# Kernel optimization log

Hardware: AMD Instinct MI355X
Metric: run time of the kernel (lower is better)

The kernel has to match this reference:

```python
import jax, jax.numpy as jnp
import numpy as np

N_NODES = 100000
N_EDGES = 1600000
MUL = 32            # channel multiplicity for every irrep
INV_SQRT_MUL = 1.0 / np.sqrt(32.0)
# path constants: wigner-3j norms (1/sqrt3 for 0x1->1 and 1x1->0, 1/sqrt6 for 1x1->1)
# combined with fan-in path normalization (fan=32 for 0e out, fan=64 for 1o out, 2 paths)
C_DOT = 1.0 / np.sqrt(3.0 * 32.0)
C_SCL = 1.0 / np.sqrt(3.0 * 64.0)
C_CRS = 1.0 / np.sqrt(6.0 * 64.0)


def setup_inputs() -> dict:
    key = jax.random.key(0)
    ks = jax.random.split(key, 12)
    x = jax.random.normal(ks[0], (N_NODES, 128), jnp.float32)
    pos = jax.random.normal(ks[1], (N_NODES, 3), jnp.float32)
    edge_index = jax.random.randint(ks[2], (2, N_EDGES), 0, N_NODES, jnp.int32)
    # o3.Linear(32x0e+32x1o -> 32x0e+32x0e+32x1o): per-irrep channel mixing
    W_node_s = jax.random.normal(ks[3], (32, 64), jnp.float32)   # 0e -> (scalars|gates)
    W_node_v = jax.random.normal(ks[4], (32, 32), jnp.float32)   # 1o -> 1o
    # FullyConnectedTensorProduct(32x0e+32x1o, 1x1o -> 32x0e+32x1o): 3 CG paths
    W_tp_d = jax.random.normal(ks[5], (32, 32), jnp.float32)     # 1o x 1o -> 0e (dot)
    W_tp_s = jax.random.normal(ks[6], (32, 32), jnp.float32)     # 0e x 1o -> 1o
    W_tp_c = jax.random.normal(ks[7], (32, 32), jnp.float32)     # 1o x 1o -> 1o (cross)
    # o3.Linear(32x0e+32x1o -> 32x0e+32x1o)
    W_msg_s = jax.random.normal(ks[8], (32, 32), jnp.float32)
    W_msg_v = jax.random.normal(ks[9], (32, 32), jnp.float32)
    ln_gamma = jnp.ones((128,), jnp.float32)
    ln_beta = jnp.zeros((128,), jnp.float32)
    return {"x": x, "pos": pos, "edge_index": edge_index,
            "W_node_s": W_node_s, "W_node_v": W_node_v,
            "W_tp_d": W_tp_d, "W_tp_s": W_tp_s, "W_tp_c": W_tp_c,
            "W_msg_s": W_msg_s, "W_msg_v": W_msg_v,
            "ln_gamma": ln_gamma, "ln_beta": ln_beta}


def reference(x, pos, edge_index, W_node_s, W_node_v, W_tp_d, W_tp_s, W_tp_c,
              W_msg_s, W_msg_v, ln_gamma, ln_beta):
    N = x.shape[0]
    row, col = edge_index[0], edge_index[1]
    # split node irreps: 32 scalars (0e) | 32 vectors (1o) of dim 3
    s = x[:, :32]                       # [N,32]
    v = x[:, 32:].reshape(-1, 32, 3)    # [N,32,3]
    # lin_node (equivariant linear, path-normalized by 1/sqrt(fan_in)=1/sqrt(32))
    h_s = (s @ W_node_s) * INV_SQRT_MUL                          # [N,64]
    h_v = jnp.einsum('nid,ij->njd', v, W_node_v) * INV_SQRT_MUL  # [N,32,3]
    # Gate: relu scalars, sigmoid gates multiply the gated vectors
    sc = jax.nn.relu(h_s[:, :32])                                # [N,32]
    hv = h_v * jax.nn.sigmoid(h_s[:, 32:])[:, :, None]           # [N,32,3]
    # spherical harmonics l=1, component norm: sqrt(3)*unit vec in e3nn (y,z,x) order
    rel = pos[col] - pos[row]                                    # [E,3]
    unit = rel / jnp.sqrt(jnp.sum(rel * rel, -1, keepdims=True) + 1e-12)
    u = jnp.sqrt(3.0) * unit[:, (1, 2, 0)]                       # [E,3]
    # gather source-node features per edge
    sj = sc[col]                                                 # [E,32]
    vj = hv[col]                                                 # [E,32,3]
    # CG tensor product paths
    dot = jnp.einsum('eid,ed->ei', vj, u)                        # 1o x 1o -> 0e
    crs = jnp.cross(vj, u[:, None, :])                           # 1o x 1o -> 1o
    m0 = (dot @ W_tp_d) * C_DOT                                  # [E,32]
    m1 = (sj @ W_tp_s)[:, :, None] * u[:, None, :] * C_SCL \
         + jnp.einsum('eid,ik->ekd', crs, W_tp_c) * C_CRS        # [E,32,3]
    m = jnp.concatenate([m0, m1.reshape(-1, 96)], -1)            # [E,128]
    # scatter-mean over destination nodes (row)
    deg = jax.ops.segment_sum(jnp.ones_like(row, jnp.float32), row,
                              num_segments=N).clip(1.0)
    mi = jax.ops.segment_sum(m, row, num_segments=N) / deg[:, None]
    # lin_msg
    ms = (mi[:, :32] @ W_msg_s) * INV_SQRT_MUL
    mv = jnp.einsum('nid,ij->njd', mi[:, 32:].reshape(-1, 32, 3),
                    W_msg_v) * INV_SQRT_MUL
    o = jnp.concatenate([ms, mv.reshape(-1, 96)], -1)            # [N,128]
    # LayerNorm over 128 dims (as in the original, affine)
    mu = o.mean(-1, keepdims=True)
    var = o.var(-1, keepdims=True)
    o = (o - mu) / jnp.sqrt(var + 1e-5) * ln_gamma + ln_beta
    return x + o
```

## Files before the change

kernel.cpp:

```cpp
#include <hip/hip_runtime.h>
#include <math.h>


static constexpr float INV_SQRT_MUL = 0.17677669529663687f;
static constexpr float C_DOT = 0.10206207261596575f;
static constexpr float C_SCL = 0.07216878364870322f;
static constexpr float C_CRS = 0.05103103630798288f;
static constexpr float SQRT3 = 1.7320508075688772f;
static constexpr int MAXDEG = 48;

#define WS_ALIGN(x) (((x) + 255) & ~(size_t)255)

__device__ __forceinline__ unsigned short f2bf(float v) {
    unsigned int b = __float_as_uint(v);
    b += 0x7FFFu + ((b >> 16) & 1u);
    return (unsigned short)(b >> 16);
}
__device__ __forceinline__ float bf2f(unsigned short u) {
    return __uint_as_float(((unsigned int)u) << 16);
}

__global__ __launch_bounds__(1024)
void fuse_weights(const float* __restrict__ Wtpd, const float* __restrict__ Wtps,
                  const float* __restrict__ Wtpc, const float* __restrict__ Wms,
                  const float* __restrict__ Wmv,
                  float* __restrict__ Wds, float* __restrict__ Wsv, float* __restrict__ Wcv) {
    int t = threadIdx.x;
    int i = t >> 5, j = t & 31;
    float a = 0.f, b = 0.f, c = 0.f;
#pragma unroll
    for (int k = 0; k < 32; ++k) {
        a += Wtpd[i * 32 + k] * Wms[k * 32 + j];
        b += Wtps[i * 32 + k] * Wmv[k * 32 + j];
        c += Wtpc[i * 32 + k] * Wmv[k * 32 + j];
    }
    Wds[t] = a * (C_DOT * INV_SQRT_MUL);
    Wsv[t] = b * (C_SCL * INV_SQRT_MUL);
    Wcv[t] = c * (C_CRS * INV_SQRT_MUL);
}

__global__ __launch_bounds__(128)
void node_feat_scatter(const float* __restrict__ x, const float* __restrict__ Wns,
                       const float* __restrict__ Wnv, unsigned short* __restrict__ feat,
                       const int* __restrict__ eidx, int* __restrict__ cnt,
                       int* __restrict__ slots, int N, int E) {
    int t = threadIdx.x;
    float w[32], wg[32];
    int d = 0, pidx;
    if (t < 32) {
        pidx = t * 4;
#pragma unroll
        for (int k = 0; k < 32; ++k) w[k] = Wns[k * 64 + t];
    } else {
        int cc = t - 32; d = cc >> 5; int i = cc & 31;
        pidx = i * 4 + 1 + d;
#pragma unroll
        for (int k = 0; k < 32; ++k) { w[k] = Wnv[k * 32 + i]; wg[k] = Wns[k * 64 + 32 + i]; }
    }
    __shared__ float xs[128];
    for (int n = blockIdx.x; n < N; n += gridDim.x) {
        xs[t] = x[(size_t)n * 128 + t];
        __syncthreads();
        float val;
        if (t < 32) {
            float h = 0.f;
#pragma unroll
            for (int k = 0; k < 32; ++k) h += xs[k] * w[k];
            val = fmaxf(h * INV_SQRT_MUL, 0.f);
        } else {
            float h = 0.f, g = 0.f;
#pragma unroll
            for (int k = 0; k < 32; ++k) { h += xs[32 + k * 3 + d] * w[k]; g += xs[k] * wg[k]; }
            float sig = 1.f / (1.f + expf(-g * INV_SQRT_MUL));
            val = h * INV_SQRT_MUL * sig;
        }
        feat[(size_t)n * 128 + pidx] = f2bf(val);
        __syncthreads();
    }
    for (int e = blockIdx.x * 128 + t; e < E; e += gridDim.x * 128) {
        int r = eidx[e];
        int c = eidx[E + e];
        int p = atomicAdd(&cnt[r], 1);
        if (p < MAXDEG) __builtin_nontemporal_store(c, &slots[(size_t)r * MAXDEG + p]);
    }
}

__global__ __launch_bounds__(256)
void agg_kernel(const float* __restrict__ x, const float* __restrict__ pos,
                const ushort4* __restrict__ feat, const int* __restrict__ cnt,
                const int* __restrict__ slots,
                const float* __restrict__ Wds, const float* __restrict__ Wsv,
                const float* __restrict__ Wcv, const float* __restrict__ gamma,
                const float* __restrict__ beta, float* __restrict__ out, int N) {
    int t = threadIdx.x;
    int hw = t >> 5;
    int lane = t & 31;
    int n = blockIdx.x * 8 + hw;
    bool live = (n < N);

    __shared__ float4 cu[8][MAXDEG];
    __shared__ float4 finA[8][32];
    __shared__ float4 finB[8][32];

    int deg = live ? cnt[n] : 0;
    int c = min(deg, MAXDEG);

    float prx = 0.f, pry = 0.f, prz = 0.f;
    if (live) { prx = pos[n * 3 + 0]; pry = pos[n * 3 + 1]; prz = pos[n * 3 + 2]; }

    if (lane < c) {
        int col = slots[(size_t)n * MAXDEG + lane];
        float rx = pos[col * 3 + 0] - prx;
        float ry = pos[col * 3 + 1] - pry;
        float rz = pos[col * 3 + 2] - prz;
        float inv = rsqrtf(rx * rx + ry * ry + rz * rz + 1e-12f) * SQRT3;
        cu[hw][lane] = make_float4(ry * inv, rz * inv, rx * inv, __int_as_float(col));
    }
    if (c > 32 && lane < c - 32) {
        int col = slots[(size_t)n * MAXDEG + 32 + lane];
        float rx = pos[col * 3 + 0] - prx;
        float ry = pos[col * 3 + 1] - pry;
        float rz = pos[col * 3 + 2] - prz;
        float inv = rsqrtf(rx * rx + ry * ry + rz * rz + 1e-12f) * SQRT3;
        cu[hw][32 + lane] = make_float4(ry * inv, rz * inv, rx * inv, __int_as_float(col));
    }
    __syncthreads();

    float D = 0.f, S0 = 0.f, S1 = 0.f, S2 = 0.f, C0 = 0.f, C1 = 0.f, C2 = 0.f;
    for (int j = 0; j < c; ++j) {
        float4 q = cu[hw][j];
        int col = __float_as_int(q.w);
        ushort4 f = feat[(size_t)col * 32 + lane];
        float sj = bf2f(f.x);
        float h0 = bf2f(f.y), h1 = bf2f(f.z), h2 = bf2f(f.w);
        float u0 = q.x, u1 = q.y, u2 = q.z;
        D  += h0 * u0 + h1 * u1 + h2 * u2;
        S0 += sj * u0; S1 += sj * u1; S2 += sj * u2;
        C0 += h1 * u2 - h2 * u1;
        C1 += h2 * u0 - h0 * u2;
        C2 += h0 * u1 - h1 * u0;
    }
    finA[hw][lane] = make_float4(D, S0, S1, S2);
    finB[hw][lane] = make_float4(C0, C1, C2, 0.f);
    __syncthreads();

    float invdeg = 1.0f / ((deg > 0) ? (float)deg : 1.0f);
    float a0 = 0.f, aV0 = 0.f, aV1 = 0.f, aV2 = 0.f;
#pragma unroll 8
    for (int i = 0; i < 32; ++i) {
        float4 a = finA[hw][i];
        float4 b = finB[hw][i];
        float wd = Wds[i * 32 + lane];
        float ws = Wsv[i * 32 + lane];
        float wc = Wcv[i * 32 + lane];
        a0  += a.x * wd;
        aV0 += a.y * ws + b.x * wc;
        aV1 += a.z * ws + b.y * wc;
        aV2 += a.w * ws + b.z * wc;
    }
    float vd = a0 * invdeg;
    float v0 = aV0 * invdeg, v1 = aV1 * invdeg, v2 = aV2 * invdeg;

    float s1 = vd + v0 + v1 + v2;
    float s2 = vd * vd + v0 * v0 + v1 * v1 + v2 * v2;
#pragma unroll
    for (int m = 16; m >= 1; m >>= 1) {
        s1 += __shfl_xor(s1, m);
        s2 += __shfl_xor(s2, m);
    }
    float mu = s1 * (1.f / 128.f);
    float var = s2 * (1.f / 128.f) - mu * mu;
    float rstd = rsqrtf(var + 1e-5f);

    if (live) {
        size_t base = (size_t)n * 128;
        int chv = 32 + lane * 3;
        float xv0 = __builtin_nontemporal_load(&x[base + lane]);
        float xa  = __builtin_nontemporal_load(&x[base + chv + 0]);
        float xb  = __builtin_nontemporal_load(&x[base + chv + 1]);
        float xc  = __builtin_nontemporal_load(&x[base + chv + 2]);
        __builtin_nontemporal_store(xv0 + (vd - mu) * rstd * gamma[lane] + beta[lane], &out[base + lane]);
        __builtin_nontemporal_store(xa + (v0 - mu) * rstd * gamma[chv + 0] + beta[chv + 0], &out[base + chv + 0]);
        __builtin_nontemporal_store(xb + (v1 - mu) * rstd * gamma[chv + 1] + beta[chv + 1], &out[base + chv + 1]);
        __builtin_nontemporal_store(xc + (v2 - mu) * rstd * gamma[chv + 2] + beta[chv + 2], &out[base + chv + 2]);
    }
}

extern "C" void kernel_launch(void* const* d_in, const int* in_sizes, int n_in,
                              void* d_out, int out_size, void* d_ws, size_t ws_size,
                              hipStream_t stream) {
    const float* x     = (const float*)d_in[0];
    const float* pos   = (const float*)d_in[1];
    const int*   eidx  = (const int*)d_in[2];
    const float* Wns   = (const float*)d_in[3];
    const float* Wnv   = (const float*)d_in[4];
    const float* Wtpd  = (const float*)d_in[5];
    const float* Wtps  = (const float*)d_in[6];
    const float* Wtpc  = (const float*)d_in[7];
    const float* Wms   = (const float*)d_in[8];
    const float* Wmv   = (const float*)d_in[9];
    const float* gamma = (const float*)d_in[10];
    const float* beta  = (const float*)d_in[11];
    float* out = (float*)d_out;

    int N = in_sizes[0] / 128;
    int E = in_sizes[2] / 2;

    char* ws = (char*)d_ws;
    size_t off = 0;
    unsigned short* feat = (unsigned short*)(ws + off); off += WS_ALIGN((size_t)N * 128 * 2);
    int*   slots    = (int*)(ws + off);   off += WS_ALIGN((size_t)N * MAXDEG * 4);
    int*   cnt      = (int*)(ws + off);   off += WS_ALIGN((size_t)N * 4);
    float* Wds      = (float*)(ws + off); off += WS_ALIGN(1024 * 4);
    float* Wsv      = (float*)(ws + off); off += WS_ALIGN(1024 * 4);
    float* Wcv      = (float*)(ws + off); off += WS_ALIGN(1024 * 4);

    hipMemsetAsync(cnt, 0, (size_t)N * 4, stream);

    fuse_weights<<<1, 1024, 0, stream>>>(Wtpd, Wtps, Wtpc, Wms, Wmv, Wds, Wsv, Wcv);
    node_feat_scatter<<<4096, 128, 0, stream>>>(x, Wns, Wnv, feat, eidx, cnt, slots, N, E);
    agg_kernel<<<(N + 7) / 8, 256, 0, stream>>>(x, pos, (const ushort4*)feat, cnt, slots,
                                                Wds, Wsv, Wcv, gamma, beta, out, N);
}
```

Measured before the change: 393.2 us.

## Precompute edge unit vectors in scatter, split feature and scatter blocks

The scatter phase now computes each edge's scaled unit direction and stores it with the column index as a float4 slot, so the aggregation kernel reads the bucket directly instead of gathering pos again. Feature and scatter work now run on separate block ranges of one launch so they overlap. The memset is fused into the weight-fusion launch, and the fused weights are staged in LDS. This quadruples slot storage (16B per slot) and depends on workspace size, with a fallback thin path when space is short.

```diff
diff --git a/kernel.cpp b/kernel.cpp
--- a/kernel.cpp
+++ b/kernel.cpp
@@ -8,6 +8,8 @@
 static constexpr float C_CRS = 0.05103103630798288f;
 static constexpr float SQRT3 = 1.7320508075688772f;
 static constexpr int MAXDEG = 48;
+static constexpr int FEAT_B = 2048;
+static constexpr int SCAT_B = 2048;
 
 #define WS_ALIGN(x) (((x) + 255) & ~(size_t)255)
 
@@ -21,80 +23,215 @@
 }
 
 __global__ __launch_bounds__(1024)
-void fuse_weights(const float* __restrict__ Wtpd, const float* __restrict__ Wtps,
-                  const float* __restrict__ Wtpc, const float* __restrict__ Wms,
-                  const float* __restrict__ Wmv,
-                  float* __restrict__ Wds, float* __restrict__ Wsv, float* __restrict__ Wcv) {
+void fuse_zero(const float* __restrict__ Wtpd, const float* __restrict__ Wtps,
+               const float* __restrict__ Wtpc, const float* __restrict__ Wms,
+               const float* __restrict__ Wmv, float* __restrict__ Wall,
+               int* __restrict__ cnt, int N) {
     int t = threadIdx.x;
-    int i = t >> 5, j = t & 31;
-    float a = 0.f, b = 0.f, c = 0.f;
-#pragma unroll
-    for (int k = 0; k < 32; ++k) {
-        a += Wtpd[i * 32 + k] * Wms[k * 32 + j];
-        b += Wtps[i * 32 + k] * Wmv[k * 32 + j];
-        c += Wtpc[i * 32 + k] * Wmv[k * 32 + j];
-    }
-    Wds[t] = a * (C_DOT * INV_SQRT_MUL);
-    Wsv[t] = b * (C_SCL * INV_SQRT_MUL);
-    Wcv[t] = c * (C_CRS * INV_SQRT_MUL);
-}
-
+    if (blockIdx.x == 0) {
+        int i = t >> 5, j = t & 31;
+        float a = 0.f, b = 0.f, c = 0.f;
+#pragma unroll
+        for (int k = 0; k < 32; ++k) {
+            a += Wtpd[i * 32 + k] * Wms[k * 32 + j];
+            b += Wtps[i * 32 + k] * Wmv[k * 32 + j];
+            c += Wtpc[i * 32 + k] * Wmv[k * 32 + j];
+        }
+        Wall[t]        = a * (C_DOT * INV_SQRT_MUL);
+        Wall[1024 + t] = b * (C_SCL * INV_SQRT_MUL);
+        Wall[2048 + t] = c * (C_CRS * INV_SQRT_MUL);
+    } else {
+        int i = (blockIdx.x - 1) * 1024 + t;
+        if (i < N) cnt[i] = 0;
+    }
+}
+
+template <bool FAT>
 __global__ __launch_bounds__(128)
-void node_feat_scatter(const float* __restrict__ x, const float* __restrict__ Wns,
-                       const float* __restrict__ Wnv, unsigned short* __restrict__ feat,
-                       const int* __restrict__ eidx, int* __restrict__ cnt,
-                       int* __restrict__ slots, int N, int E) {
+void phase1(const float* __restrict__ x, const float* __restrict__ Wns,
+            const float* __restrict__ Wnv, const float* __restrict__ pos,
+            const int* __restrict__ eidx, unsigned short* __restrict__ feat,
+            int* __restrict__ cnt, void* __restrict__ slots_raw, int N, int E) {
     int t = threadIdx.x;
-    float w[32], wg[32];
-    int d = 0, pidx;
-    if (t < 32) {
-        pidx = t * 4;
-#pragma unroll
-        for (int k = 0; k < 32; ++k) w[k] = Wns[k * 64 + t];
+    if (blockIdx.x < FEAT_B) {
+        float w[32], wg[32];
+        int d = 0, pidx;
+        if (t < 32) {
+            pidx = t * 4;
+#pragma unroll
+            for (int k = 0; k < 32; ++k) w[k] = Wns[k * 64 + t];
+        } else {
+            int cc = t - 32; d = cc >> 5; int i = cc & 31;
+            pidx = i * 4 + 1 + d;
+#pragma unroll
+            for (int k = 0; k < 32; ++k) { w[k] = Wnv[k * 32 + i]; wg[k] = Wns[k * 64 + 32 + i]; }
+        }
+        __shared__ float xs[128];
+        for (int n = blockIdx.x; n < N; n += FEAT_B) {
+            xs[t] = x[(size_t)n * 128 + t];
+            __syncthreads();
+            float val;
+            if (t < 32) {
+                float h = 0.f;
+#pragma unroll
+                for (int k = 0; k < 32; ++k) h += xs[k] * w[k];
+                val = fmaxf(h * INV_SQRT_MUL, 0.f);
+            } else {
+                float h = 0.f, g = 0.f;
+#pragma unroll
+                for (int k = 0; k < 32; ++k) { h += xs[32 + k * 3 + d] * w[k]; g += xs[k] * wg[k]; }
+                float sig = 1.f / (1.f + expf(-g * INV_SQRT_MUL));
+                val = h * INV_SQRT_MUL * sig;
+            }
+            feat[(size_t)n * 128 + pidx] = f2bf(val);
+            __syncthreads();
+        }
     } else {
-        int cc = t - 32; d = cc >> 5; int i = cc & 31;
-        pidx = i * 4 + 1 + d;
-#pragma unroll
-        for (int k = 0; k < 32; ++k) { w[k] = Wnv[k * 32 + i]; wg[k] = Wns[k * 64 + 32 + i]; }
-    }
-    __shared__ float xs[128];
-    for (int n = blockIdx.x; n < N; n += gridDim.x) {
-        xs[t] = x[(size_t)n * 128 + t];
-        __syncthreads();
-        float val;
-        if (t < 32) {
-            float h = 0.f;
-#pragma unroll
-            for (int k = 0; k < 32; ++k) h += xs[k] * w[k];
-            val = fmaxf(h * INV_SQRT_MUL, 0.f);
-        } else {
-            float h = 0.f, g = 0.f;
-#pragma unroll
-            for (int k = 0; k < 32; ++k) { h += xs[32 + k * 3 + d] * w[k]; g += xs[k] * wg[k]; }
-            float sig = 1.f / (1.f + expf(-g * INV_SQRT_MUL));
-            val = h * INV_SQRT_MUL * sig;
-        }
-        feat[(size_t)n * 128 + pidx] = f2bf(val);
-        __syncthreads();
-    }
-    for (int e = blockIdx.x * 128 + t; e < E; e += gridDim.x * 128) {
-        int r = eidx[e];
-        int c = eidx[E + e];
-        int p = atomicAdd(&cnt[r], 1);
-        if (p < MAXDEG) __builtin_nontemporal_store(c, &slots[(size_t)r * MAXDEG + p]);
+        int tid = (blockIdx.x - FEAT_B) * 128 + t;
+        int Q = E >> 2;
+        const int4* r4p = (const int4*)eidx;
+        const int4* c4p = (const int4*)(eidx + E);
+        float4* slotsF = (float4*)slots_raw;
+        int*    slotsI = (int*)slots_raw;
+        for (int q = tid; q < Q; q += SCAT_B * 128) {
+            int4 R = r4p[q];
+            int4 C = c4p[q];
+            int rr[4] = {R.x, R.y, R.z, R.w};
+            int cc[4] = {C.x, C.y, C.z, C.w};
+            if (FAT) {
+                float prx[4], pry[4], prz[4], pcx[4], pcy[4], pcz[4];
+#pragma unroll
+                for (int k = 0; k < 4; ++k) {
+                    prx[k] = pos[rr[k] * 3 + 0]; pry[k] = pos[rr[k] * 3 + 1]; prz[k] = pos[rr[k] * 3 + 2];
+                    pcx[k] = pos[cc[k] * 3 + 0]; pcy[k] = pos[cc[k] * 3 + 1]; pcz[k] = pos[cc[k] * 3 + 2];
+                }
+#pragma unroll
+                for (int k = 0; k < 4; ++k) {
+                    float rx = pcx[k] - prx[k], ry = pcy[k] - pry[k], rz = pcz[k] - prz[k];
+                    float inv = rsqrtf(rx * rx + ry * ry + rz * rz + 1e-12f) * SQRT3;
+                    int p = atomicAdd(&cnt[rr[k]], 1);
+                    if (p < MAXDEG)
+                        slotsF[(size_t)rr[k] * MAXDEG + p] =
+                            make_float4(ry * inv, rz * inv, rx * inv, __int_as_float(cc[k]));
+                }
+            } else {
+#pragma unroll
+                for (int k = 0; k < 4; ++k) {
+                    int p = atomicAdd(&cnt[rr[k]], 1);
+                    if (p < MAXDEG) slotsI[(size_t)rr[k] * MAXDEG + p] = cc[k];
+                }
+            }
+        }
+        for (int e = (Q << 2) + tid; e < E; e += SCAT_B * 128) {
+            int r = eidx[e], c = eidx[E + e];
+            int p = atomicAdd(&cnt[r], 1);
+            if (p < MAXDEG) {
+                if (FAT) {
+                    float rx = pos[c * 3 + 0] - pos[r * 3 + 0];
+                    float ry = pos[c * 3 + 1] - pos[r * 3 + 1];
+                    float rz = pos[c * 3 + 2] - pos[r * 3 + 2];
+                    float inv = rsqrtf(rx * rx + ry * ry + rz * rz + 1e-12f) * SQRT3;
+                    slotsF[(size_t)r * MAXDEG + p] = make_float4(ry * inv, rz * inv, rx * inv, __int_as_float(c));
+                } else {
+                    slotsI[(size_t)r * MAXDEG + p] = c;
+                }
+            }
+        }
     }
 }
 
 __global__ __launch_bounds__(256)
-void agg_kernel(const float* __restrict__ x, const float* __restrict__ pos,
-                const ushort4* __restrict__ feat, const int* __restrict__ cnt,
-                const int* __restrict__ slots,
-                const float* __restrict__ Wds, const float* __restrict__ Wsv,
-                const float* __restrict__ Wcv, const float* __restrict__ gamma,
-                const float* __restrict__ beta, float* __restrict__ out, int N) {
+void agg_fat(const float* __restrict__ x, const ushort4* __restrict__ feat,
+             const int* __restrict__ cnt, const float4* __restrict__ slots,
+             const float* __restrict__ Wall, const float* __restrict__ gamma,
+             const float* __restrict__ beta, float* __restrict__ out, int N) {
     int t = threadIdx.x;
-    int hw = t >> 5;
-    int lane = t & 31;
+    __shared__ float wlds[3072];
+    __shared__ float4 finA[8][32];
+    __shared__ float4 finB[8][32];
+    {
+        float4* w4 = (float4*)wlds;
+        const float4* g4 = (const float4*)Wall;
+        for (int i = t; i < 768; i += 256) w4[i] = g4[i];
+    }
+    int hw = t >> 5, lane = t & 31;
+    int n = blockIdx.x * 8 + hw;
+    bool live = (n < N);
+    int deg = live ? cnt[n] : 0;
+    int c = min(deg, MAXDEG);
+    const float4* bucket = slots + (size_t)(live ? n : 0) * MAXDEG;
+
+    float D = 0.f, S0 = 0.f, S1 = 0.f, S2 = 0.f, C0 = 0.f, C1 = 0.f, C2 = 0.f;
+    auto body = [&](int j) {
+        float4 q = bucket[j];
+        int col = __float_as_int(q.w);
+        ushort4 f = feat[(size_t)col * 32 + lane];
+        float sj = bf2f(f.x);
+        float h0 = bf2f(f.y), h1 = bf2f(f.z), h2 = bf2f(f.w);
+        D  += h0 * q.x + h1 * q.y + h2 * q.z;
+        S0 += sj * q.x; S1 += sj * q.y; S2 += sj * q.z;
+        C0 += h1 * q.z - h2 * q.y;
+        C1 += h2 * q.x - h0 * q.z;
+        C2 += h0 * q.y - h1 * q.x;
+    };
+    int j = 0;
+    for (; j + 3 < c; j += 4) { body(j); body(j + 1); body(j + 2); body(j + 3); }
+    for (; j < c; ++j) body(j);
+
+    finA[hw][lane] = make_float4(D, S0, S1, S2);
+    finB[hw][lane] = make_float4(C0, C1, C2, 0.f);
+    __syncthreads();
+
+    float invdeg = 1.0f / (float)((deg > 0) ? deg : 1);
+    float a0 = 0.f, aV0 = 0.f, aV1 = 0.f, aV2 = 0.f;
+#pragma unroll 8
+    for (int i = 0; i < 32; ++i) {
+        float4 a = finA[hw][i];
+        float4 b = finB[hw][i];
+        float wd = wlds[i * 32 + lane];
+        float ws = wlds[1024 + i * 32 + lane];
+        float wc = wlds[2048 + i * 32 + lane];
+        a0  += a.x * wd;
+        aV0 += a.y * ws + b.x * wc;
+        aV1 += a.z * ws + b.y * wc;
+        aV2 += a.w * ws + b.z * wc;
+    }
+    float vd = a0 * invdeg;
+    float v0 = aV0 * invdeg, v1 = aV1 * invdeg, v2 = aV2 * invdeg;
+
+    float s1 = vd + v0 + v1 + v2;
+    float s2 = vd * vd + v0 * v0 + v1 * v1 + v2 * v2;
+#pragma unroll
+    for (int m = 16; m >= 1; m >>= 1) {
+        s1 += __shfl_xor(s1, m);
+        s2 += __shfl_xor(s2, m);
+    }
+    float mu = s1 * (1.f / 128.f);
+    float var = s2 * (1.f / 128.f) - mu * mu;
+    float rstd = rsqrtf(var + 1e-5f);
+
+    if (live) {
+        size_t base = (size_t)n * 128;
+        int chv = 32 + lane * 3;
+        float xv0 = __builtin_nontemporal_load(&x[base + lane]);
+        float xa  = __builtin_nontemporal_load(&x[base + chv + 0]);
+        float xb  = __builtin_nontemporal_load(&x[base + chv + 1]);
+        float xc  = __builtin_nontemporal_load(&x[base + chv + 2]);
+        __builtin_nontemporal_store(xv0 + (vd - mu) * rstd * gamma[lane] + beta[lane], &out[base + lane]);
+        __builtin_nontemporal_store(xa + (v0 - mu) * rstd * gamma[chv + 0] + beta[chv + 0], &out[base + chv + 0]);
+        __builtin_nontemporal_store(xb + (v1 - mu) * rstd * gamma[chv + 1] + beta[chv + 1], &out[base + chv + 1]);
+        __builtin_nontemporal_store(xc + (v2 - mu) * rstd * gamma[chv + 2] + beta[chv + 2], &out[base + chv + 2]);
+    }
+}
+
+__global__ __launch_bounds__(256)
+void agg_thin(const float* __restrict__ x, const float* __restrict__ pos,
+              const ushort4* __restrict__ feat, const int* __restrict__ cnt,
+              const int* __restrict__ slots, const float* __restrict__ Wall,
+              const float* __restrict__ gamma, const float* __restrict__ beta,
+              float* __restrict__ out, int N) {
+    int t = threadIdx.x;
+    int hw = t >> 5, lane = t & 31;
     int n = blockIdx.x * 8 + hw;
     bool live = (n < N);
 
@@ -110,17 +247,13 @@
 
     if (lane < c) {
         int col = slots[(size_t)n * MAXDEG + lane];
-        float rx = pos[col * 3 + 0] - prx;
-        float ry = pos[col * 3 + 1] - pry;
-        float rz = pos[col * 3 + 2] - prz;
+        float rx = pos[col * 3 + 0] - prx, ry = pos[col * 3 + 1] - pry, rz = pos[col * 3 + 2] - prz;
         float inv = rsqrtf(rx * rx + ry * ry + rz * rz + 1e-12f) * SQRT3;
         cu[hw][lane] = make_float4(ry * inv, rz * inv, rx * inv, __int_as_float(col));
     }
     if (c > 32 && lane < c - 32) {
         int col = slots[(size_t)n * MAXDEG + 32 + lane];
-        float rx = pos[col * 3 + 0] - prx;
-        float ry = pos[col * 3 + 1] - pry;
-        float rz = pos[col * 3 + 2] - prz;
+        float rx = pos[col * 3 + 0] - prx, ry = pos[col * 3 + 1] - pry, rz = pos[col * 3 + 2] - prz;
         float inv = rsqrtf(rx * rx + ry * ry + rz * rz + 1e-12f) * SQRT3;
         cu[hw][32 + lane] = make_float4(ry * inv, rz * inv, rx * inv, __int_as_float(col));
     }
@@ -133,26 +266,25 @@
         ushort4 f = feat[(size_t)col * 32 + lane];
         float sj = bf2f(f.x);
         float h0 = bf2f(f.y), h1 = bf2f(f.z), h2 = bf2f(f.w);
-        float u0 = q.x, u1 = q.y, u2 = q.z;
-        D  += h0 * u0 + h1 * u1 + h2 * u2;
-        S0 += sj * u0; S1 += sj * u1; S2 += sj * u2;
-        C0 += h1 * u2 - h2 * u1;
-        C1 += h2 * u0 - h0 * u2;
-        C2 += h0 * u1 - h1 * u0;
+        D  += h0 * q.x + h1 * q.y + h2 * q.z;
+        S0 += sj * q.x; S1 += sj * q.y; S2 += sj * q.z;
+        C0 += h1 * q.z - h2 * q.y;
+        C1 += h2 * q.x - h0 * q.z;
+        C2 += h0 * q.y - h1 * q.x;
     }
     finA[hw][lane] = make_float4(D, S0, S1, S2);
     finB[hw][lane] = make_float4(C0, C1, C2, 0.f);
     __syncthreads();
 
-    float invdeg = 1.0f / ((deg > 0) ? (float)deg : 1.0f);
+    float invdeg = 1.0f / (float)((deg > 0) ? deg : 1);
     float a0 = 0.f, aV0 = 0.f, aV1 = 0.f, aV2 = 0.f;
 #pragma unroll 8
     for (int i = 0; i < 32; ++i) {
         float4 a = finA[hw][i];
         float4 b = finB[hw][i];
-        float wd = Wds[i * 32 + lane];
-        float ws = Wsv[i * 32 + lane];
-        float wc = Wcv[i * 32 + lane];
+        float wd = Wall[i * 32 + lane];
+        float ws = Wall[1024 + i * 32 + lane];
+        float wc = Wall[2048 + i * 32 + lane];
         a0  += a.x * wd;
         aV0 += a.y * ws + b.x * wc;
         aV1 += a.z * ws + b.y * wc;
@@ -209,16 +341,21 @@
     char* ws = (char*)d_ws;
     size_t off = 0;
     unsigned short* feat = (unsigned short*)(ws + off); off += WS_ALIGN((size_t)N * 128 * 2);
-    int*   slots    = (int*)(ws + off);   off += WS_ALIGN((size_t)N * MAXDEG * 4);
-    int*   cnt      = (int*)(ws + off);   off += WS_ALIGN((size_t)N * 4);
-    float* Wds      = (float*)(ws + off); off += WS_ALIGN(1024 * 4);
-    float* Wsv      = (float*)(ws + off); off += WS_ALIGN(1024 * 4);
-    float* Wcv      = (float*)(ws + off); off += WS_ALIGN(1024 * 4);
-
-    hipMemsetAsync(cnt, 0, (size_t)N * 4, stream);
-
-    fuse_weights<<<1, 1024, 0, stream>>>(Wtpd, Wtps, Wtpc, Wms, Wmv, Wds, Wsv, Wcv);
-    node_feat_scatter<<<4096, 128, 0, stream>>>(x, Wns, Wnv, feat, eidx, cnt, slots, N, E);
-    agg_kernel<<<(N + 7) / 8, 256, 0, stream>>>(x, pos, (const ushort4*)feat, cnt, slots,
-                                                Wds, Wsv, Wcv, gamma, beta, out, N);
-}
+    int*   cnt  = (int*)(ws + off);   off += WS_ALIGN((size_t)N * 4);
+    float* Wall = (float*)(ws + off); off += WS_ALIGN(3072 * 4);
+    void*  slots = (void*)(ws + off);
+    size_t fat_need = off + WS_ALIGN((size_t)N * MAXDEG * 16);
+    bool fat = (fat_need <= ws_size);
+
+    int zb = 1 + (N + 1023) / 1024;
+    fuse_zero<<<zb, 1024, 0, stream>>>(Wtpd, Wtps, Wtpc, Wms, Wmv, Wall, cnt, N);
+    if (fat) {
+        phase1<true><<<FEAT_B + SCAT_B, 128, 0, stream>>>(x, Wns, Wnv, pos, eidx, feat, cnt, slots, N, E);
+        agg_fat<<<(N + 7) / 8, 256, 0, stream>>>(x, (const ushort4*)feat, cnt, (const float4*)slots,
+                                                 Wall, gamma, beta, out, N);
+    } else {
+        phase1<false><<<FEAT_B + SCAT_B, 128, 0, stream>>>(x, Wns, Wnv, pos, eidx, feat, cnt, slots, N, E);
+        agg_thin<<<(N + 7) / 8, 256, 0, stream>>>(x, pos, (const ushort4*)feat, cnt, (const int*)slots,
+                                                  Wall, gamma, beta, out, N);
+    }
+}
```

New measurement: 378.1 us. -3.8%, faster.
